# Optimization experiments

Measured on AMD Instinct MI355X. Metric: run time of the kernel, lower is better.

The kernel has to match this reference:

```python
import jax, jax.numpy as jnp
import numpy as np

DIM = 512
HEADS = 8
DIM_HEAD = 64
INNER = HEADS * DIM_HEAD  # 512
SCALE = DIM_HEAD ** -0.5


def setup_inputs() -> dict:
    key = jax.random.key(0)
    k1, k2, k3, k4 = jax.random.split(key, 4)
    x = jax.random.normal(k1, (4, 2048, DIM), dtype=jnp.float32)
    # Dense(inner_dim*3, use_bias=False): weight [dim, 3*inner]
    w_qkv = jax.random.normal(k2, (DIM, 3 * INNER), dtype=jnp.float32) * (DIM ** -0.5)
    # to_out Dense(dim): weight [inner, dim] + bias [dim]
    w_out = jax.random.normal(k3, (INNER, DIM), dtype=jnp.float32) * (INNER ** -0.5)
    b_out = jax.random.normal(k4, (DIM,), dtype=jnp.float32) * 0.01
    return {"x": x, "w_qkv": w_qkv, "w_out": w_out, "b_out": b_out}


def reference(x, w_qkv, w_out, b_out):
    b, n, _ = x.shape
    qkv = x @ w_qkv                                  # [b, n, 3*inner]
    q, k, v = jnp.split(qkv, 3, axis=-1)             # each [b, n, inner]
    def to_heads(t):
        return t.reshape(b, n, HEADS, DIM_HEAD).transpose(0, 2, 1, 3)  # [b, h, n, d]
    q, k, v = map(to_heads, (q, k, v))
    dots = jnp.einsum('bhid,bhjd->bhij', q, k) * SCALE
    attn = jax.nn.softmax(dots, axis=-1)
    out = jnp.einsum('bhij,bhjd->bhid', attn, v)     # [b, h, n, d]
    out = out.transpose(0, 2, 1, 3).reshape(b, n, INNER)
    return out @ w_out + b_out                       # [b, n, dim]
```

## Files before the change

kernel.cpp:

```cpp
#include <hip/hip_runtime.h>
#include <stdint.h>

#define DIM    512
#define HEADS  8
#define DHEAD  64
#define SEQ    2048
#define BATCH  4
#define BH     (BATCH*HEADS)
#define MROWS  (BATCH*SEQ)
#define NQKV   (3*DIM)
#define QSCALE 0.18033688011112042f

typedef __bf16 bf16x8 __attribute__((ext_vector_type(8)));
typedef float  f32x4  __attribute__((ext_vector_type(4)));

typedef unsigned short u16;

__device__ __forceinline__ u16 f2bf(float f) {
    union { float f; uint32_t u; } v; v.f = f;
    uint32_t u = v.u;
    uint32_t r = (u + 0x7FFFu + ((u >> 16) & 1u)) >> 16;
    return (u16)r;
}
__device__ __forceinline__ float bf2f(u16 h) {
    union { uint32_t u; float f; } v; v.u = ((uint32_t)h) << 16;
    return v.f;
}
__device__ __forceinline__ uint32_t pk2bf(float a, float b) {
    return (uint32_t)f2bf(a) | ((uint32_t)f2bf(b) << 16);
}

__device__ __forceinline__ void async16(const void* g, u16* l) {
    __builtin_amdgcn_global_load_lds(
        (const __attribute__((address_space(1))) void*)g,
        (__attribute__((address_space(3))) void*)l, 16, 0, 0);
}

__global__ void detect_dtype(const u16* __restrict__ x, int* __restrict__ flag) {
    __shared__ int cnt;
    if (threadIdx.x == 0) cnt = 0;
    __syncthreads();
    u16 v = x[threadIdx.x * 2];
    int e = (v >> 7) & 0xFF;
    int ok = (v == 0) || (e >= 100 && e <= 140);
    atomicAdd(&cnt, ok);
    __syncthreads();
    if (threadIdx.x == 0) *flag = (cnt >= 192) ? 1 : 0;
}

__global__ void pack_x(const void* __restrict__ xin, const int* __restrict__ flag,
                       u16* __restrict__ xb) {
    int i = blockIdx.x * 256 + threadIdx.x;
    int isbf = *flag;
    if (isbf) {
        ((uint2*)xb)[i] = ((const uint2*)xin)[i];
    } else {
        float4 v = ((const float4*)xin)[i];
        ushort4 o;
        o.x = f2bf(v.x); o.y = f2bf(v.y); o.z = f2bf(v.z); o.w = f2bf(v.w);
        ((ushort4*)xb)[i] = o;
    }
}

__global__ void pack_wt(const void* __restrict__ win, const int* __restrict__ flag,
                        u16* __restrict__ wt, int K, int N) {
    int idx = blockIdx.x * 256 + threadIdx.x;
    if (idx >= K * N) return;
    int k = idx / N, n = idx - k * N;
    int isbf = *flag;
    u16 v = isbf ? ((const u16*)win)[idx] : f2bf(((const float*)win)[idx]);
    wt[(size_t)n * K + k] = v;
}

template<int KDIM, int TM, int TN>
__device__ __forceinline__ void gemm_lds(
        const u16* __restrict__ A, const u16* __restrict__ Bt,
        int m0, int n0, int tid, u16* As, u16* Bs,
        f32x4 (&acc)[TM / 32][TN / 32]) {
    int lane = tid & 63, ln = lane & 15, quad = lane >> 4, w = tid >> 6;
    int wm = (w >> 1) * (TM / 2), wn = (w & 1) * (TN / 2);

    auto stage = [&](int k0) {
#pragma unroll
        for (int ii = 0; ii < TM / 64; ++ii) {
            int r0 = (ii * 4 + w) * 16;
            int row = r0 + (lane >> 2);
            int seg = (lane & 3) ^ (row & 3);
            async16(A + (size_t)(m0 + row) * KDIM + k0 + seg * 8, As + r0 * 32);
        }
#pragma unroll
        for (int ii = 0; ii < TN / 64; ++ii) {
            int r0 = (ii * 4 + w) * 16;
            int row = r0 + (lane >> 2);
            int seg = (lane & 3) ^ (row & 3);
            async16(Bt + (size_t)(n0 + row) * KDIM + k0 + seg * 8, Bs + r0 * 32);
        }
    };

    stage(0);
#pragma unroll 1
    for (int kk = 0; kk < KDIM / 32; ++kk) {
        __syncthreads();
        bf16x8 a[TM / 32], b[TN / 32];
        int rseg = (quad ^ (ln & 3)) * 8;
#pragma unroll
        for (int i = 0; i < TM / 32; ++i)
            a[i] = *(const bf16x8*)(As + (wm + i * 16 + ln) * 32 + rseg);
#pragma unroll
        for (int j = 0; j < TN / 32; ++j)
            b[j] = *(const bf16x8*)(Bs + (wn + j * 16 + ln) * 32 + rseg);
#pragma unroll
        for (int i = 0; i < TM / 32; ++i)
#pragma unroll
            for (int j = 0; j < TN / 32; ++j)
                acc[i][j] = __builtin_amdgcn_mfma_f32_16x16x32_bf16(
                    a[i], b[j], acc[i][j], 0, 0, 0);
        __syncthreads();
        if (kk + 1 < KDIM / 32) stage((kk + 1) * 32);
    }
}

__global__ __launch_bounds__(256, 3) void qkv_gemm(
        const u16* __restrict__ X, const u16* __restrict__ Wt,
        u16* __restrict__ Qb, u16* __restrict__ Kb, u16* __restrict__ Vt) {
    __shared__ __align__(16) u16 As[128 * 32];
    __shared__ __align__(16) u16 Bs[128 * 32];

    int tid  = threadIdx.x;
    int lane = tid & 63, ln = lane & 15, quad = lane >> 4, wid = tid >> 6;
    int m0 = blockIdx.x * 128, n0 = blockIdx.y * 128;
    int wm = (wid >> 1) * 64, wn = (wid & 1) * 64;

    f32x4 acc[4][4];
#pragma unroll
    for (int i = 0; i < 4; ++i)
#pragma unroll
        for (int j = 0; j < 4; ++j) acc[i][j] = 0.f;

    gemm_lds<DIM, 128, 128>(X, Wt, m0, n0, tid, As, Bs, acc);

#pragma unroll
    for (int j = 0; j < 4; ++j) {
        int col   = n0 + wn + j * 16 + ln;
        int which = col >> 9;
        int hd    = col & 511;
        int h     = hd >> 6, d = hd & 63;
#pragma unroll
        for (int i = 0; i < 4; ++i) {
            int rbase = m0 + wm + i * 16 + quad * 4;
#pragma unroll
            for (int r = 0; r < 4; ++r) {
                int row = rbase + r;
                int b = row >> 11, n = row & 2047;
                int bh = b * HEADS + h;
                if (which == 0)
                    Qb[((size_t)bh * SEQ + n) * DHEAD + d] = f2bf(acc[i][j][r] * QSCALE);
                else if (which == 1)
                    Kb[((size_t)bh * SEQ + n) * DHEAD + d] = f2bf(acc[i][j][r]);
                else
                    Vt[((size_t)bh * DHEAD + d) * SEQ + n] = f2bf(acc[i][j][r]);
            }
        }
    }
}

__global__ __launch_bounds__(256, 2) void flash_attn(
        const u16* __restrict__ Qb, const u16* __restrict__ Kb,
        const u16* __restrict__ Vt, u16* __restrict__ Ob) {
    __shared__ __align__(16) u16 Kc[2][64 * 64];
    __shared__ __align__(16) u16 Vc[2][64 * 64];
    __shared__ __align__(16) u16 Pl[4][32 * 64];

    int tid  = threadIdx.x;
    int lane = tid & 63, ln = lane & 15, quad = lane >> 4, wid = tid >> 6;
    int bh = blockIdx.x;
    int q0 = blockIdx.y * 128 + wid * 32;

    const u16* Qh = Qb + (size_t)bh * SEQ * DHEAD;
    const u16* Kh = Kb + (size_t)bh * SEQ * DHEAD;
    const u16* Vh = Vt + (size_t)bh * DHEAD * SEQ;

    int srow = lane >> 3;
    int gseg = (lane & 7) ^ srow;

    auto stageKV = [&](int buf, int kc) {
#pragma unroll
        for (int ii = 0; ii < 2; ++ii) {
            int slab = wid + ii * 4;
            const u16* gk = Kh + (size_t)(kc + slab * 8 + srow) * DHEAD + gseg * 8;
            async16(gk, &Kc[buf][slab * 8 * 64]);
            const u16* gv = Vh + (size_t)(slab * 8 + srow) * SEQ + kc + gseg * 8;
            async16(gv, &Vc[buf][slab * 8 * 64]);
        }
    };

    bf16x8 qf[2][2];
#pragma unroll
    for (int qt = 0; qt < 2; ++qt)
#pragma unroll
        for (int s = 0; s < 2; ++s)
            qf[qt][s] = *(const bf16x8*)(
                Qh + (size_t)(q0 + qt * 16 + ln) * DHEAD + s * 32 + quad * 8);

    f32x4 o[2][4];
#pragma unroll
    for (int qt = 0; qt < 2; ++qt)
#pragma unroll
        for (int t = 0; t < 4; ++t) o[qt][t] = 0.f;
    float lsum[2] = {0.f, 0.f};

    stageKV(0, 0);
    __syncthreads();

#pragma unroll 1
    for (int kc = 0; kc < SEQ; kc += 64) {
        int cur = (kc >> 6) & 1;
        if (kc + 64 < SEQ) stageKV(cur ^ 1, kc + 64);

        bf16x8 kf[4][2], vf[4][2];
#pragma unroll
        for (int kt = 0; kt < 4; ++kt) {
            int row = kt * 16 + ln;
#pragma unroll
            for (int s = 0; s < 2; ++s) {
                int seg = (s * 4 + quad) ^ (ln & 7);
                kf[kt][s] = *(const bf16x8*)&Kc[cur][row * 64 + seg * 8];
                vf[kt][s] = *(const bf16x8*)&Vc[cur][row * 64 + seg * 8];
            }
        }

        f32x4 st[4][2];
#pragma unroll
        for (int kt = 0; kt < 4; ++kt)
#pragma unroll
            for (int qt = 0; qt < 2; ++qt) st[kt][qt] = 0.f;
#pragma unroll
        for (int kt = 0; kt < 4; ++kt)
#pragma unroll
            for (int qt = 0; qt < 2; ++qt)
#pragma unroll
                for (int s = 0; s < 2; ++s)
                    st[kt][qt] = __builtin_amdgcn_mfma_f32_16x16x32_bf16(
                        kf[kt][s], qf[qt][s], st[kt][qt], 0, 0, 0);

#pragma unroll
        for (int kt = 0; kt < 4; ++kt)
#pragma unroll
            for (int qt = 0; qt < 2; ++qt)
#pragma unroll
                for (int r = 0; r < 4; ++r) {
                    float p = exp2f(st[kt][qt][r]);
                    st[kt][qt][r] = p;
                    lsum[qt] += p;
                }

#pragma unroll
        for (int qt = 0; qt < 2; ++qt)
#pragma unroll
            for (int kt = 0; kt < 4; ++kt) {
                uint2 d;
                d.x = pk2bf(st[kt][qt][0], st[kt][qt][1]);
                d.y = pk2bf(st[kt][qt][2], st[kt][qt][3]);
                int seg = (kt * 2 + (quad >> 1)) ^ (ln & 7);
                *(uint2*)&Pl[wid][(qt * 16 + ln) * 64 + seg * 8 + (quad & 1) * 4] = d;
            }

        bf16x8 pf[2][2];
#pragma unroll
        for (int qt = 0; qt < 2; ++qt)
#pragma unroll
            for (int s = 0; s < 2; ++s) {
                int seg = (s * 4 + quad) ^ (ln & 7);
                pf[qt][s] = *(const bf16x8*)&Pl[wid][(qt * 16 + ln) * 64 + seg * 8];
            }

#pragma unroll
        for (int t = 0; t < 4; ++t)
#pragma unroll
            for (int s = 0; s < 2; ++s)
#pragma unroll
                for (int qt = 0; qt < 2; ++qt)
                    o[qt][t] = __builtin_amdgcn_mfma_f32_16x16x32_bf16(
                        pf[qt][s], vf[t][s], o[qt][t], 0, 0, 0);

        __syncthreads();
    }

#pragma unroll
    for (int qt = 0; qt < 2; ++qt) {
        float s = lsum[qt];
        s += __shfl_xor(s, 16);
        s += __shfl_xor(s, 32);
        lsum[qt] = 1.0f / s;
    }

    int b = bh >> 3, h = bh & 7;
#pragma unroll
    for (int qt = 0; qt < 2; ++qt) {
#pragma unroll
        for (int t = 0; t < 4; ++t) {
            int d = t * 16 + ln;
#pragma unroll
            for (int r = 0; r < 4; ++r) {
                int qrow = quad * 4 + r;
                float inv = __shfl(lsum[qt], qrow);
                int n = q0 + qt * 16 + qrow;
                Ob[((size_t)(b * SEQ + n)) * DIM + h * DHEAD + d] =
                    f2bf(o[qt][t][r] * inv);
            }
        }
    }
}

__global__ __launch_bounds__(256, 3) void out_gemm(
        const u16* __restrict__ A, const u16* __restrict__ Wt,
        const void* __restrict__ bias, void* __restrict__ out,
        const int* __restrict__ flag) {
    __shared__ __align__(16) u16 As[64 * 32];
    __shared__ __align__(16) u16 Bs[128 * 32];

    int tid  = threadIdx.x;
    int lane = tid & 63, ln = lane & 15, quad = lane >> 4, wid = tid >> 6;
    int m0 = blockIdx.x * 64, n0 = blockIdx.y * 128;
    int wm = (wid >> 1) * 32, wn = (wid & 1) * 64;
    int isbf = *flag;

    f32x4 acc[2][4];
#pragma unroll
    for (int i = 0; i < 2; ++i)
#pragma unroll
        for (int j = 0; j < 4; ++j) acc[i][j] = 0.f;

    gemm_lds<DIM, 64, 128>(A, Wt, m0, n0, tid, As, Bs, acc);

#pragma unroll
    for (int j = 0; j < 4; ++j) {
        int col = n0 + wn + j * 16 + ln;
        float bv = isbf ? bf2f(((const u16*)bias)[col])
                        : ((const float*)bias)[col];
#pragma unroll
        for (int i = 0; i < 2; ++i) {
            int rbase = m0 + wm + i * 16 + quad * 4;
#pragma unroll
            for (int r = 0; r < 4; ++r) {
                int row = rbase + r;
                size_t off = (size_t)row * DIM + col;
                float val = acc[i][j][r] + bv;
                if (isbf) ((u16*)out)[off] = f2bf(val);
                else      ((float*)out)[off] = val;
            }
        }
    }
}

extern "C" void kernel_launch(void* const* d_in, const int* in_sizes, int n_in,
                              void* d_out, int out_size, void* d_ws, size_t ws_size,
                              hipStream_t stream) {
    const void* x     = d_in[0];
    const void* w_qkv = d_in[1];
    const void* w_out = d_in[2];
    const void* b_out = d_in[3];

    int* flag   = (int*)d_ws;
    u16* x_bf   = (u16*)((char*)d_ws + 16);
    u16* wt_qkv = x_bf + (size_t)MROWS * DIM;
    u16* wt_out = wt_qkv + (size_t)NQKV * DIM;
    u16* Qb     = wt_out + (size_t)DIM * DIM;
    u16* Kb     = Qb + (size_t)BH * SEQ * DHEAD;
    u16* Vt     = Kb + (size_t)BH * SEQ * DHEAD;
    u16* attn   = x_bf;

    detect_dtype<<<1, 256, 0, stream>>>((const u16*)x, flag);
    pack_x<<<(MROWS * DIM / 4) / 256, 256, 0, stream>>>(x, flag, x_bf);
    pack_wt<<<(DIM * NQKV + 255) / 256, 256, 0, stream>>>(w_qkv, flag, wt_qkv, DIM, NQKV);
    pack_wt<<<(DIM * DIM + 255) / 256, 256, 0, stream>>>(w_out, flag, wt_out, DIM, DIM);
    qkv_gemm<<<dim3(MROWS / 128, NQKV / 128), 256, 0, stream>>>(x_bf, wt_qkv, Qb, Kb, Vt);
    flash_attn<<<dim3(BH, SEQ / 128), 256, 0, stream>>>(Qb, Kb, Vt, attn);
    out_gemm<<<dim3(MROWS / 64, DIM / 128), 256, 0, stream>>>(attn, wt_out, b_out, d_out, flag);
}
```

Before: 204.4 us.

## Use fast exp2, cheaper bf16 packing, vectorized V stores, padded P layout

Replaces exp2f with the hardware exp2 builtin and fuses the exponent with packing of P into LDS. pk2bf now rounds half-up and packs with a single perm instead of two round-to-nearest-even conversions. The V-transpose epilogue writes four consecutive sequence elements as one 8-byte store instead of four scalar stores. The P scratch buffer switches from an XOR swizzle to a padded stride of 80 elements. Together these aim to cut ALU and store instructions in the softmax and epilogue, at a small cost in bf16 rounding accuracy and extra LDS.

```diff
diff --git a/kernel.cpp b/kernel.cpp
--- a/kernel.cpp
+++ b/kernel.cpp
@@ -16,6 +16,12 @@
 
 typedef unsigned short u16;
 
+#if __has_builtin(__builtin_amdgcn_exp2f)
+#define EXP2(x) __builtin_amdgcn_exp2f(x)
+#else
+#define EXP2(x) exp2f(x)
+#endif
+
 __device__ __forceinline__ u16 f2bf(float f) {
     union { float f; uint32_t u; } v; v.f = f;
     uint32_t u = v.u;
@@ -27,7 +33,12 @@
     return v.f;
 }
 __device__ __forceinline__ uint32_t pk2bf(float a, float b) {
-    return (uint32_t)f2bf(a) | ((uint32_t)f2bf(b) << 16);
+    union { float f; uint32_t u; } ua, ub; ua.f = a; ub.f = b;
+#if __has_builtin(__builtin_amdgcn_perm)
+    return __builtin_amdgcn_perm(ub.u + 0x8000u, ua.u + 0x8000u, 0x07060302u);
+#else
+    return ((ua.u + 0x8000u) >> 16) | ((ub.u + 0x8000u) & 0xFFFF0000u);
+#endif
 }
 
 __device__ __forceinline__ void async16(const void* g, u16* l) {
@@ -148,28 +159,36 @@
 #pragma unroll
         for (int i = 0; i < 4; ++i) {
             int rbase = m0 + wm + i * 16 + quad * 4;
-#pragma unroll
-            for (int r = 0; r < 4; ++r) {
-                int row = rbase + r;
-                int b = row >> 11, n = row & 2047;
+            if (which == 2) {
+                int b = rbase >> 11, n = rbase & 2047;
                 int bh = b * HEADS + h;
-                if (which == 0)
-                    Qb[((size_t)bh * SEQ + n) * DHEAD + d] = f2bf(acc[i][j][r] * QSCALE);
-                else if (which == 1)
-                    Kb[((size_t)bh * SEQ + n) * DHEAD + d] = f2bf(acc[i][j][r]);
-                else
-                    Vt[((size_t)bh * DHEAD + d) * SEQ + n] = f2bf(acc[i][j][r]);
-            }
-        }
-    }
-}
-
+                uint2 pv;
+                pv.x = pk2bf(acc[i][j][0], acc[i][j][1]);
+                pv.y = pk2bf(acc[i][j][2], acc[i][j][3]);
+                *(uint2*)&Vt[((size_t)bh * DHEAD + d) * SEQ + n] = pv;
+            } else {
+#pragma unroll
+                for (int r = 0; r < 4; ++r) {
+                    int row = rbase + r;
+                    int b = row >> 11, n = row & 2047;
+                    int bh = b * HEADS + h;
+                    if (which == 0)
+                        Qb[((size_t)bh * SEQ + n) * DHEAD + d] = f2bf(acc[i][j][r] * QSCALE);
+                    else
+                        Kb[((size_t)bh * SEQ + n) * DHEAD + d] = f2bf(acc[i][j][r]);
+                }
+            }
+        }
+    }
+}
+
+#define PSTRIDE 80
 __global__ __launch_bounds__(256, 2) void flash_attn(
         const u16* __restrict__ Qb, const u16* __restrict__ Kb,
         const u16* __restrict__ Vt, u16* __restrict__ Ob) {
     __shared__ __align__(16) u16 Kc[2][64 * 64];
     __shared__ __align__(16) u16 Vc[2][64 * 64];
-    __shared__ __align__(16) u16 Pl[4][32 * 64];
+    __shared__ __align__(16) u16 Pl[4][32 * PSTRIDE];
 
     int tid  = threadIdx.x;
     int lane = tid & 63, ln = lane & 15, quad = lane >> 4, wid = tid >> 6;
@@ -244,35 +263,27 @@
                         kf[kt][s], qf[qt][s], st[kt][qt], 0, 0, 0);
 
 #pragma unroll
-        for (int kt = 0; kt < 4; ++kt)
-#pragma unroll
-            for (int qt = 0; qt < 2; ++qt)
-#pragma unroll
-                for (int r = 0; r < 4; ++r) {
-                    float p = exp2f(st[kt][qt][r]);
-                    st[kt][qt][r] = p;
-                    lsum[qt] += p;
-                }
-
-#pragma unroll
         for (int qt = 0; qt < 2; ++qt)
 #pragma unroll
             for (int kt = 0; kt < 4; ++kt) {
+                float p0 = EXP2(st[kt][qt][0]);
+                float p1 = EXP2(st[kt][qt][1]);
+                float p2 = EXP2(st[kt][qt][2]);
+                float p3 = EXP2(st[kt][qt][3]);
+                lsum[qt] += (p0 + p1) + (p2 + p3);
                 uint2 d;
-                d.x = pk2bf(st[kt][qt][0], st[kt][qt][1]);
-                d.y = pk2bf(st[kt][qt][2], st[kt][qt][3]);
-                int seg = (kt * 2 + (quad >> 1)) ^ (ln & 7);
-                *(uint2*)&Pl[wid][(qt * 16 + ln) * 64 + seg * 8 + (quad & 1) * 4] = d;
+                d.x = pk2bf(p0, p1);
+                d.y = pk2bf(p2, p3);
+                *(uint2*)&Pl[wid][(qt * 16 + ln) * PSTRIDE + kt * 16 + quad * 4] = d;
             }
 
         bf16x8 pf[2][2];
 #pragma unroll
         for (int qt = 0; qt < 2; ++qt)
 #pragma unroll
-            for (int s = 0; s < 2; ++s) {
-                int seg = (s * 4 + quad) ^ (ln & 7);
-                pf[qt][s] = *(const bf16x8*)&Pl[wid][(qt * 16 + ln) * 64 + seg * 8];
-            }
+            for (int s = 0; s < 2; ++s)
+                pf[qt][s] = *(const bf16x8*)
+                    &Pl[wid][(qt * 16 + ln) * PSTRIDE + s * 32 + quad * 8];
 
 #pragma unroll
         for (int t = 0; t < 4; ++t)
```

After: 182.3 us. 10.8% less time.
